# Kernel tuning notes

Measured on AMD Instinct MI355X. Metric: run time of the kernel, lower is better.

## Reference

```python
import jax, jax.numpy as jnp
from jax import lax
import numpy as np


def conv2d(x, w, b=None, stride=1, padding=0, groups=1, dilation=1):
    out = lax.conv_general_dilated(
        x, w, (stride, stride), [(padding, padding)] * 2,
        rhs_dilation=(dilation, dilation), feature_group_count=groups,
        dimension_numbers=('NCHW', 'OIHW', 'NCHW'))
    return out if b is None else out + b[None, :, None, None]


def unfold1d(x, k, axis):
    # torch.nn.functional.unfold with kernel (k,1) or (1,k), pad k//2 on that axis.
    # Returns [B, C, k, H, W] (channel-major, kernel-tap inner), matching torch layout.
    pad = k // 2
    pads = [(0, 0)] * 4
    pads[axis] = (pad, pad)
    xp = jnp.pad(x, pads)
    return jnp.stack([lax.slice_in_dim(xp, i, i + x.shape[axis], axis=axis)
                      for i in range(k)], axis=2)


def ikba(x, att, k, g, b_cb, w_cb):
    # Per-pixel dynamic grouped conv: attention mixes nset codebook kernels,
    # applied as vertical (k,1) then horizontal (1,k) unfold-matmul-fold.
    B, c, H, W = x.shape
    nset = att.shape[1]
    cg = c // g
    P = H * W
    a = att.reshape(B, nset, P).transpose(0, 2, 1)          # [B,P,nset]
    bias = a @ b_cb[0]                                      # [B,P,c]
    attk = a @ w_cb[0]                                      # [B,P, 2*c*cg*k]
    half = attk.shape[-1] // 2
    ah = attk[..., :half].reshape(B, P, g, cg, cg * k)
    aw = attk[..., half:].reshape(B, P, g, cg, cg * k)
    # vertical pass
    ufh = unfold1d(x, k, 2).reshape(B, g, cg * k, P).transpose(0, 3, 1, 2)  # [B,P,g,cg*k]
    xh = jnp.einsum('bpgij,bpgj->bpgi', ah, ufh).reshape(B, P, c)
    xh = xh.transpose(0, 2, 1).reshape(B, c, H, W)
    # horizontal pass
    ufw = unfold1d(xh, k, 3).reshape(B, g, cg * k, P).transpose(0, 3, 1, 2)
    xw = jnp.einsum('bpgij,bpgj->bpgi', aw, ufw).reshape(B, P, c) + bias
    return xw.transpose(0, 2, 1).reshape(B, c, H, W)


def hff_forward(x, dw1_w, dw2_w, proj_w, lka0_w, lkas_w, lka1_w, lka1_b,
                sca_w, sca_b, c1a_w, c1b_w, c2a_w, c2a_b, c2b_w, c2b_b,
                c211_w, c211_b, w_cb, b_cb, attgamma, ga1):
    C = x.shape[1]
    K, GC = 3, 4
    g = C // GC
    sca = conv2d(jnp.mean(x, axis=(2, 3), keepdims=True), sca_w, sca_b)
    x1 = conv2d(conv2d(x, dw1_w), dw2_w, padding=1, groups=C)
    lka = conv2d(conv2d(conv2d(x, lka0_w, padding=2, groups=C),
                        lkas_w, padding=9, groups=C, dilation=3), lka1_w, lka1_b)
    t = conv2d(x, c2a_w, c2a_b, padding=1, groups=c2a_w.shape[0])
    t1, t2 = jnp.split(t, 2, axis=1)  # SimpleGate
    att = conv2d(t1 * t2, c2b_w, c2b_b) * attgamma + conv2d(x, c211_w, c211_b)
    uf = conv2d(conv2d(x, c1a_w), c1b_w, padding=1, groups=C)
    x2 = ikba(uf, att, K, g, b_cb, w_cb) * ga1 + uf
    return conv2d(x1 * x2 * sca * lka, proj_w)


def setup_inputs() -> dict:
    key = jax.random.key(0)
    ks = jax.random.split(key, 24)
    B, C, H, W = 2, 256, 64, 64
    nset, k, gc = 128, 3, 4
    g = C // gc
    cg = C // g
    def rn(i, shape, scale=0.02):
        return jax.random.normal(ks[i], shape, jnp.float32) * scale
    return {
        'x': jax.random.normal(ks[0], (B, C, H, W), jnp.float32),
        'dw1_w': rn(1, (C, C, 1, 1)),
        'dw2_w': rn(2, (C, 1, 3, 3), 0.1),
        'proj_w': rn(3, (C, C, 1, 1)),
        'lka0_w': rn(4, (C, 1, 5, 5), 0.1),
        'lkas_w': rn(5, (C, 1, 7, 7), 0.1),
        'lka1_w': rn(6, (C, C, 1, 1)),
        'lka1_b': rn(7, (C,)),
        'sca_w': rn(8, (C, C, 1, 1)),
        'sca_b': rn(9, (C,)),
        'c1a_w': rn(10, (C, C, 1, 1)),
        'c1b_w': rn(11, (C, 1, 3, 3), 0.1),
        'c2a_w': rn(12, (32, C // 32, 3, 3), 0.1),
        'c2a_b': rn(13, (32,)),
        'c2b_w': rn(14, (nset, 16, 1, 1), 0.1),
        'c2b_b': rn(15, (nset,)),
        'c211_w': rn(16, (nset, C, 1, 1)),
        'c211_b': rn(17, (nset,)),
        'w_cb': rn(18, (1, nset, C * cg * k * 2), 0.05),
        'b_cb': rn(19, (1, nset, C), 0.05),
        'attgamma': jnp.full((1, nset, 1, 1), 0.01, jnp.float32),
        'ga1': jnp.full((1, C, 1, 1), 0.01, jnp.float32),
    }


def reference(x, dw1_w, dw2_w, proj_w, lka0_w, lkas_w, lka1_w, lka1_b,
              sca_w, sca_b, c1a_w, c1b_w, c2a_w, c2a_b, c2b_w, c2b_b,
              c211_w, c211_b, w_cb, b_cb, attgamma, ga1):
    return hff_forward(x, dw1_w, dw2_w, proj_w, lka0_w, lkas_w, lka1_w, lka1_b,
                       sca_w, sca_b, c1a_w, c1b_w, c2a_w, c2a_b, c2b_w, c2b_b,
                       c211_w, c211_b, w_cb, b_cb, attgamma, ga1)
```

## Files before the change

kernel.cpp:

```cpp
#include <hip/hip_runtime.h>
#include <cstddef>

#define P_ 4096
#define HW_ 64

typedef __bf16 bf16x8 __attribute__((ext_vector_type(8)));
typedef float f32x4 __attribute__((ext_vector_type(4)));

__device__ inline ushort f2bf(float f) {
  unsigned u = __float_as_uint(f);
  unsigned r = (u + 0x7FFFu + ((u >> 16) & 1u)) >> 16;
  return (ushort)r;
}
__device__ inline float bf2f(ushort h) {
  return __uint_as_float(((unsigned)h) << 16);
}
__device__ inline unsigned pack2(ushort a, ushort b) {
  return (unsigned)a | ((unsigned)b << 16);
}

__global__ __launch_bounds__(256) void prep_mean_kernel(
    const float* __restrict__ w_cb, const float* __restrict__ dw1_w,
    const float* __restrict__ lka1_w, const float* __restrict__ c1a_w,
    const float* __restrict__ proj_w, const float* __restrict__ c211_w,
    const float* __restrict__ b_cb, ushort* __restrict__ wT,
    ushort* __restrict__ W5h, ushort* __restrict__ W5l,
    ushort* __restrict__ bth, ushort* __restrict__ btl,
    const float* __restrict__ x, float* __restrict__ mean) {
  __shared__ float T[128][65];
  int blk = blockIdx.x;
  int t = threadIdx.x;
  if (blk < 96) {
    int c0 = blk * 64;
#pragma unroll
    for (int i = 0; i < 32; ++i) {
      int l = i * 256 + t;
      int n = l >> 6, c = l & 63;
      T[n][c] = w_cb[(size_t)n * 6144 + c0 + c];
    }
    __syncthreads();
#pragma unroll
    for (int i = 0; i < 4; ++i) {
      int l = i * 256 + t;
      int c = l >> 4, n8 = (l & 15) << 3;
      ushort v[8];
#pragma unroll
      for (int u = 0; u < 8; ++u) v[u] = f2bf(T[n8 + u][c]);
      *(uint4*)&wT[(size_t)(c0 + c) * 128 + n8] = *(uint4*)v;
    }
  } else if (blk < 240) {
    int f = (blk - 96) * 2048 + t * 8;
    const float* srcs[5] = {dw1_w, lka1_w, c1a_w, proj_w, c211_w};
    const int base[6] = {0, 65536, 131072, 196608, 262144, 294912};
    int r = 0;
    while (f >= base[r + 1]) ++r;
    const float* s = srcs[r] + (f - base[r]);
    float4 a = *(const float4*)s;
    float4 b4 = *(const float4*)(s + 4);
    float vv[8] = {a.x, a.y, a.z, a.w, b4.x, b4.y, b4.z, b4.w};
    ushort vh[8], vl[8];
#pragma unroll
    for (int u = 0; u < 8; ++u) {
      ushort h = f2bf(vv[u]);
      vh[u] = h;
      vl[u] = f2bf(vv[u] - bf2f(h));
    }
    *(uint4*)&W5h[f] = *(uint4*)vh;
    *(uint4*)&W5l[f] = *(uint4*)vl;
  } else if (blk < 244) {
    int c0 = (blk - 240) * 64;
#pragma unroll
    for (int i = 0; i < 32; ++i) {
      int l = i * 256 + t;
      int n = l >> 6, c = l & 63;
      T[n][c] = b_cb[(size_t)n * 256 + c0 + c];
    }
    __syncthreads();
#pragma unroll
    for (int i = 0; i < 4; ++i) {
      int l = i * 256 + t;
      int c = l >> 4, n8 = (l & 15) << 3;
      ushort vh[8], vl[8];
#pragma unroll
      for (int u = 0; u < 8; ++u) {
        float fv = T[n8 + u][c];
        ushort h = f2bf(fv);
        vh[u] = h;
        vl[u] = f2bf(fv - bf2f(h));
      }
      *(uint4*)&bth[(size_t)(c0 + c) * 128 + n8] = *(uint4*)vh;
      *(uint4*)&btl[(size_t)(c0 + c) * 128 + n8] = *(uint4*)vl;
    }
  } else {
    int bc = blk - 244;
    const float* xp = x + (size_t)bc * P_;
    float s = 0.f;
    for (int i = t; i < P_; i += 256) s += xp[i];
    float* red = (float*)T;
    red[t] = s;
    __syncthreads();
    for (int off2 = 128; off2 > 0; off2 >>= 1) {
      if (t < off2) red[t] += red[t + off2];
      __syncthreads();
    }
    if (t == 0) mean[bc] = red[0] * (1.f / P_);
  }
}


__device__ inline void xsplit_body(const float* sb, ushort* dhb, ushort* dlb,
                                   int p0, int K, char* smem) {
  float (*T)[65] = (float(*)[65])smem;
  int t = threadIdx.x;
#pragma unroll
  for (int i = 0; i < 32; ++i) {
    int l = i * 256 + t;
    int n = l >> 6, c = l & 63;
    T[n][c] = sb[(size_t)n * P_ + p0 + c];
  }
  __syncthreads();
#pragma unroll
  for (int i = 0; i < 4; ++i) {
    int l = i * 256 + t;
    int c = l >> 4, n8 = (l & 15) << 3;
    ushort vh[8], vl[8];
#pragma unroll
    for (int u = 0; u < 8; ++u) {
      float f = T[n8 + u][c];
      ushort h = f2bf(f);
      vh[u] = h;
      vl[u] = f2bf(f - bf2f(h));
    }
    *(uint4*)&dhb[(size_t)(p0 + c) * K + n8] = *(uint4*)vh;
    *(uint4*)&dlb[(size_t)(p0 + c) * K + n8] = *(uint4*)vl;
  }
}

__device__ inline void gemm_body(const ushort* Whb, const ushort* Wlb,
                                 const ushort* Xhb, const ushort* Xlb,
                                 const float* bias, float* out, int M, int m0,
                                 int p0, int b, int K, char* smem) {
  ushort* Wsh = (ushort*)smem;
  ushort* Wsl = (ushort*)(smem + 9216);
  ushort* Xsh = (ushort*)(smem + 18432);
  ushort* Xsl = (ushort*)(smem + 27648);
  int t = threadIdx.x;
  int w = t >> 6, lane = t & 63, lm = lane & 15, lq = lane >> 4;
  f32x4 C[4];
#pragma unroll
  for (int pt = 0; pt < 4; ++pt) C[pt] = (f32x4)(0.f);
  for (int k0 = 0; k0 < K; k0 += 64) {
#pragma unroll
    for (int i = 0; i < 2; ++i) {
      int u = i * 256 + t;
      int row = u >> 3, k8 = (u & 7) * 8;
      *(uint4*)&Wsh[row * 72 + k8] = *(const uint4*)&Whb[(size_t)row * K + k0 + k8];
      *(uint4*)&Wsl[row * 72 + k8] = *(const uint4*)&Wlb[(size_t)row * K + k0 + k8];
      *(uint4*)&Xsh[row * 72 + k8] = *(const uint4*)&Xhb[(size_t)row * K + k0 + k8];
      *(uint4*)&Xsl[row * 72 + k8] = *(const uint4*)&Xlb[(size_t)row * K + k0 + k8];
    }
    __syncthreads();
#pragma unroll
    for (int kt = 0; kt < 2; ++kt) {
      bf16x8 Ah = *(const bf16x8*)&Wsh[(w * 16 + lm) * 72 + kt * 32 + lq * 8];
      bf16x8 Al = *(const bf16x8*)&Wsl[(w * 16 + lm) * 72 + kt * 32 + lq * 8];
#pragma unroll
      for (int pt = 0; pt < 4; ++pt) {
        bf16x8 Bh = *(const bf16x8*)&Xsh[(pt * 16 + lm) * 72 + kt * 32 + lq * 8];
        bf16x8 Bl = *(const bf16x8*)&Xsl[(pt * 16 + lm) * 72 + kt * 32 + lq * 8];
        C[pt] = __builtin_amdgcn_mfma_f32_16x16x32_bf16(Ah, Bh, C[pt], 0, 0, 0);
        C[pt] = __builtin_amdgcn_mfma_f32_16x16x32_bf16(Al, Bh, C[pt], 0, 0, 0);
        C[pt] = __builtin_amdgcn_mfma_f32_16x16x32_bf16(Ah, Bl, C[pt], 0, 0, 0);
      }
    }
    __syncthreads();
  }
#pragma unroll
  for (int pt = 0; pt < 4; ++pt) {
    int p = p0 + pt * 16 + lm;
#pragma unroll
    for (int r = 0; r < 4; ++r) {
      int m = m0 + w * 16 + lq * 4 + r;
      float v = C[pt][r];
      if (bias) v += bias[m];
      out[((size_t)b * M + m) * P_ + p] = v;
    }
  }
}

__global__ __launch_bounds__(256) void gemm_bf16s_kernel(
    const ushort* __restrict__ Wh, const ushort* __restrict__ Wl,
    const ushort* __restrict__ Xh, const ushort* __restrict__ Xl,
    const float* __restrict__ bias, float* __restrict__ out, int M, int K) {
  __shared__ __align__(16) char smem[36864];
  int p0 = blockIdx.x * 64, m0 = blockIdx.y * 64, b = blockIdx.z;
  gemm_body(Wh + (size_t)m0 * K, Wl + (size_t)m0 * K,
            Xh + ((size_t)b * P_ + p0) * K, Xl + ((size_t)b * P_ + p0) * K,
            bias, out, M, m0, p0, b, K, smem);
}

__global__ __launch_bounds__(256) void sca_xsplit_kernel(
    const float* __restrict__ x, ushort* __restrict__ dh,
    ushort* __restrict__ dl, const float* __restrict__ mean,
    const float* __restrict__ w, const float* __restrict__ bias,
    float* __restrict__ sca) {
  __shared__ __align__(16) char smem[33280];
  int blk = blockIdx.x;
  int t = threadIdx.x;
  if (blk < 256) {
    const int K = 256;
    int p0 = (blk & 63) * 64;
    int kb = (blk >> 6) & 1;
    int b = blk >> 7;
    xsplit_body(x + ((size_t)b * K + kb * 128) * P_,
                dh + (size_t)b * P_ * K + (size_t)kb * 128,
                dl + (size_t)b * P_ * K + (size_t)kb * 128, p0, K, smem);
  } else {
    int b = blk - 256, c = t;
    const float* mb = mean + b * 256;
    const float* wr = w + c * 256;
    float s = bias[c];
    for (int k = 0; k < 256; ++k) s += wr[k] * mb[k];
    sca[b * 256 + c] = s;
  }
}

__global__ __launch_bounds__(256) void main1_kernel(
    const ushort* __restrict__ Xh, const ushort* __restrict__ Xl,
    const ushort* __restrict__ W5h, const ushort* __restrict__ W5l,
    const float* __restrict__ c211_b, float* __restrict__ B1,
    float* __restrict__ B3, float* __restrict__ att0,
    const float* __restrict__ x, const float* __restrict__ w0,
    const float* __restrict__ w1, float* __restrict__ outlka,
    const float* __restrict__ c2aw, const float* __restrict__ c2ab,
    float* __restrict__ sgate) {
  __shared__ __align__(16) char smem[45392];
  int blk = blockIdx.x;
  int t = threadIdx.x;
  if (blk < 1280) {
    const int K = 256;
    int p = blk & 63;
    int my = (blk >> 6) % 10;
    int b = blk / 640;
    const ushort *Wh, *Wl;
    float* out;
    const float* bias = nullptr;
    int M, m0;
    if (my < 4) {
      Wh = W5h; Wl = W5l; out = B1; M = 256; m0 = my * 64;
    } else if (my < 8) {
      Wh = W5h + 131072; Wl = W5l + 131072; out = B3; M = 256; m0 = (my - 4) * 64;
    } else {
      Wh = W5h + 262144; Wl = W5l + 262144; out = att0; M = 128;
      m0 = (my - 8) * 64; bias = c211_b;
    }
    int p0 = p * 64;
    gemm_body(Wh + (size_t)m0 * K, Wl + (size_t)m0 * K,
              Xh + ((size_t)b * P_ + p0) * K, Xl + ((size_t)b * P_ + p0) * K,
              bias, out, M, m0, p0, b, K, smem);
  } else if (blk < 1792) {
    constexpr int PN0 = 68;
    constexpr int PN1 = 82;
    float* p0a = (float*)smem;
    float* p1a = (float*)(smem + PN0 * PN0 * 4);
    int bc = blk - 1280;
    const float* ib = x + (size_t)bc * P_;
    for (int i = t; i < PN0 * PN0; i += 256) p0a[i] = 0.f;
    for (int i = t; i < PN1 * PN1; i += 256) p1a[i] = 0.f;
    __syncthreads();
#pragma unroll
    for (int i = 0; i < 4; ++i) {
      int l = i * 1024 + t * 4;
      int y = l >> 6, xx = l & 63;
      float4 v = *(const float4*)(ib + l);
      float* d = &p0a[(y + 2) * PN0 + 2 + xx];
      d[0] = v.x; d[1] = v.y; d[2] = v.z; d[3] = v.w;
    }
    float wr0[25];
    {
      const float* wp = w0 + (size_t)(bc & 255) * 25;
#pragma unroll
      for (int i = 0; i < 25; ++i) wr0[i] = wp[i];
    }
    __syncthreads();
#pragma unroll
    for (int r = 0; r < 16; ++r) {
      int l = r * 256 + t;
      int y = l >> 6, xx = l & 63;
      float s = 0.f;
#pragma unroll
      for (int dy = 0; dy < 5; ++dy)
#pragma unroll
        for (int dx = 0; dx < 5; ++dx)
          s += wr0[dy * 5 + dx] * p0a[(y + dy) * PN0 + xx + dx];
      p1a[(y + 9) * PN1 + 9 + xx] = s;
    }
    float wr1[49];
    {
      const float* wp = w1 + (size_t)(bc & 255) * 49;
#pragma unroll
      for (int i = 0; i < 49; ++i) wr1[i] = wp[i];
    }
    __syncthreads();
    float* ob = outlka + (size_t)bc * P_;
#pragma unroll
    for (int r = 0; r < 16; ++r) {
      int l = r * 256 + t;
      int y = l >> 6, xx = l & 63;
      float s = 0.f;
#pragma unroll
      for (int dy = 0; dy < 7; ++dy)
#pragma unroll
        for (int dx = 0; dx < 7; ++dx)
          s += wr1[dy * 7 + dx] * p1a[(y + dy * 3) * PN1 + xx + dx * 3];
      ob[l] = s;
    }
  } else {
    int idx = (blk - 1792) * 256 + t;
    int xq = idx & 63, y = (idx >> 6) & 63, go = (idx >> 12) & 15, b = idx >> 16;
    float acc[2];
#pragma unroll
    for (int h = 0; h < 2; ++h) {
      int gc = go + h * 16;
      const float* wr = c2aw + gc * 72;
      const float* xb = x + ((size_t)b * 256 + gc * 8) * P_;
      float ss = c2ab[gc];
      for (int ci = 0; ci < 8; ++ci)
        for (int dy = 0; dy < 3; ++dy) {
          int yy = y + dy - 1;
          if (yy < 0 || yy >= 64) continue;
          for (int dx = 0; dx < 3; ++dx) {
            int xx = xq + dx - 1;
            if (xx < 0 || xx >= 64) continue;
            ss += wr[ci * 9 + dy * 3 + dx] * xb[(size_t)ci * P_ + yy * 64 + xx];
          }
        }
      acc[h] = ss;
    }
    sgate[idx] = acc[0] * acc[1];
  }
}

__global__ __launch_bounds__(256) void dwsplit_kernel(
    const float* __restrict__ in1, const float* __restrict__ w1,
    float* __restrict__ out1, const float* __restrict__ in2,
    const float* __restrict__ w2, float* __restrict__ out2,
    const float* __restrict__ B6, ushort* __restrict__ XT2h,
    ushort* __restrict__ XT2l) {
  __shared__ __align__(16) char smem[33280];
  int blk = blockIdx.x;
  int t = threadIdx.x;
  if (blk < 1024) {
    constexpr int PN = 66;
    float* pl = (float*)smem;
    int which = blk >> 9;
    int bc = blk & 511;
    const float* in = which ? in2 : in1;
    const float* w = which ? w2 : w1;
    float* out = which ? out2 : out1;
    const float* ib = in + (size_t)bc * P_;
    for (int i = t; i < PN * PN; i += 256) pl[i] = 0.f;
    __syncthreads();
#pragma unroll
    for (int i = 0; i < 4; ++i) {
      int l = i * 1024 + t * 4;
      int y = l >> 6, xx = l & 63;
      float4 v = *(const float4*)(ib + l);
      float* d = &pl[(y + 1) * PN + 1 + xx];
      d[0] = v.x; d[1] = v.y; d[2] = v.z; d[3] = v.w;
    }
    float wr[9];
    const float* wp = w + (size_t)(bc & 255) * 9;
#pragma unroll
    for (int i = 0; i < 9; ++i) wr[i] = wp[i];
    __syncthreads();
    float* ob = out + (size_t)bc * P_;
#pragma unroll
    for (int r = 0; r < 16; ++r) {
      int l = r * 256 + t;
      int y = l >> 6, xx = l & 63;
      float s = 0.f;
#pragma unroll
      for (int dy = 0; dy < 3; ++dy)
#pragma unroll
        for (int dx = 0; dx < 3; ++dx)
          s += wr[dy * 3 + dx] * pl[(y + dy) * PN + xx + dx];
      ob[l] = s;
    }
  } else {
    const int K = 256;
    int l = blk - 1024;
    int p0 = (l & 63) * 64;
    int kb = (l >> 6) & 1;
    int b = l >> 7;
    xsplit_body(B6 + ((size_t)b * K + kb * 128) * P_,
                XT2h + (size_t)b * P_ * K + (size_t)kb * 128,
                XT2l + (size_t)b * P_ * K + (size_t)kb * 128, p0, K, smem);
  }
}

__global__ __launch_bounds__(256) void gemm_c2b_kernel(
    const ushort* __restrict__ Wh, const ushort* __restrict__ Wl,
    const ushort* __restrict__ XT2h, const ushort* __restrict__ XT2l,
    const float* __restrict__ lka1_b, float* __restrict__ B1,
    const float* __restrict__ sb, const float* __restrict__ c2bw,
    const float* __restrict__ c2bb, const float* __restrict__ gamma,
    const float* __restrict__ res, ushort* __restrict__ outh,
    ushort* __restrict__ outl) {
  __shared__ __align__(16) char smem[36864];
  int my = blockIdx.y;
  int b = blockIdx.z;
  int t = threadIdx.x;
  if (my < 4) {
    const int K = 256;
    int p0 = blockIdx.x * 64, m0 = my * 64;
    gemm_body(Wh + (size_t)m0 * K, Wl + (size_t)m0 * K,
              XT2h + ((size_t)b * P_ + p0) * K, XT2l + ((size_t)b * P_ + p0) * K,
              lka1_b, B1, 256, m0, p0, b, K, smem);
  } else {
    const int K = 16, M = 128;
    int p0 = blockIdx.x * 64;
    int m0 = (my - 4) * 64;
    float (*Ws)[68] = (float(*)[68])smem;
    float (*Xs)[68] = (float(*)[68])(smem + 4352 * 4);
    int tm = t >> 4, tp = t & 15;
    float acc[4][4] = {};
    const float* inb = sb + (size_t)b * K * P_;
    {
      int kk = t >> 4, pq = (t & 15) << 2;
      float4 v = *(const float4*)(inb + (size_t)kk * P_ + p0 + pq);
      *(float4*)&Xs[kk][pq] = v;
    }
    {
      int mm = t >> 2, kq = (t & 3) << 2;
      float4 v = *(const float4*)(c2bw + (size_t)(m0 + mm) * K + kq);
      Ws[kq + 0][mm] = v.x; Ws[kq + 1][mm] = v.y;
      Ws[kq + 2][mm] = v.z; Ws[kq + 3][mm] = v.w;
    }
    __syncthreads();
#pragma unroll
    for (int kk = 0; kk < 16; ++kk) {
      const float4 wv = *(const float4*)&Ws[kk][tm << 2];
      const float4 xv = *(const float4*)&Xs[kk][tp << 2];
      const float wa[4] = {wv.x, wv.y, wv.z, wv.w};
      const float xa[4] = {xv.x, xv.y, xv.z, xv.w};
#pragma unroll
      for (int i = 0; i < 4; ++i)
#pragma unroll
        for (int j = 0; j < 4; ++j) acc[i][j] += wa[i] * xa[j];
    }
    float val[4][4];
#pragma unroll
    for (int i = 0; i < 4; ++i) {
      int m = m0 + (tm << 2) + i;
      float bv = c2bb[m], gm = gamma[m];
      float4 rv = *(const float4*)(res + ((size_t)b * M + m) * P_ + p0 + (tp << 2));
      val[i][0] = (acc[i][0] + bv) * gm + rv.x;
      val[i][1] = (acc[i][1] + bv) * gm + rv.y;
      val[i][2] = (acc[i][2] + bv) * gm + rv.z;
      val[i][3] = (acc[i][3] + bv) * gm + rv.w;
    }
#pragma unroll
    for (int j = 0; j < 4; ++j) {
      int p = p0 + (tp << 2) + j;
      ushort vh[4], vl[4];
#pragma unroll
      for (int i = 0; i < 4; ++i) {
        float f = val[i][j];
        ushort h = f2bf(f);
        vh[i] = h;
        vl[i] = f2bf(f - bf2f(h));
      }
      size_t a = ((size_t)b * P_ + p) * 128 + m0 + (tm << 2);
      uint2 hv, lv;
      hv.x = pack2(vh[0], vh[1]); hv.y = pack2(vh[2], vh[3]);
      lv.x = pack2(vl[0], vl[1]); lv.y = pack2(vl[2], vl[3]);
      *(uint2*)&outh[a] = hv;
      *(uint2*)&outl[a] = lv;
    }
  }
}

__global__ __launch_bounds__(256) void ikba_mfma_kernel(
    const float* __restrict__ in, const ushort* __restrict__ attT,
    const ushort* __restrict__ Wt, int dirH, int wofs,
    const ushort* __restrict__ bth, const ushort* __restrict__ btl,
    const float* __restrict__ uf_ep, const float* __restrict__ ga1,
    const float* __restrict__ x1, const float* __restrict__ lka,
    const float* __restrict__ sca, ushort* __restrict__ pXh,
    ushort* __restrict__ pXl, float* __restrict__ outV) {
  __shared__ float Ts[2][4][16][66];
  __shared__ float bls[64 * 17];

  int t = threadIdx.x;
  int b = blockIdx.z;
  int quad = blockIdx.y;
  int y = blockIdx.x;
  int p0 = y * 64;
  int gg = t >> 6;
  int lane = t & 63;
  int lm = lane & 15, lq = lane >> 4;
  int gi = quad * 4 + gg;
  int x = lane;

  const ushort* Wbase = Wt + ((size_t)wofs + (size_t)gi * 48) * 128;
  bf16x8 Af[3][4];
#pragma unroll
  for (int ct = 0; ct < 3; ++ct)
#pragma unroll
    for (int K = 0; K < 4; ++K)
      Af[ct][K] = *(const bf16x8*)&Wbase[(ct * 16 + lm) * 128 + K * 32 + lq * 8];

  const ushort* Ab = attT + ((size_t)b * P_ + p0) * 128;
  f32x4 Cf[3][4];
#pragma unroll
  for (int ct = 0; ct < 3; ++ct)
#pragma unroll
    for (int pt = 0; pt < 4; ++pt) Cf[ct][pt] = (f32x4)(0.f);

#pragma unroll
  for (int pt = 0; pt < 4; ++pt) {
    bf16x8 Bf[4];
#pragma unroll
    for (int K = 0; K < 4; ++K)
      Bf[K] = *(const bf16x8*)&Ab[(pt * 16 + lm) * 128 + K * 32 + lq * 8];
#pragma unroll
    for (int ct = 0; ct < 3; ++ct)
#pragma unroll
      for (int K = 0; K < 4; ++K)
        Cf[ct][pt] = __builtin_amdgcn_mfma_f32_16x16x32_bf16(
            Af[ct][K], Bf[K], Cf[ct][pt], 0, 0, 0);
  }

  if (dirH) {
    f32x4 Cb = (f32x4)(0.f);
#pragma unroll
    for (int K = 0; K < 4; ++K) {
      bf16x8 Bb = *(const bf16x8*)&Ab[(gg * 16 + lm) * 128 + K * 32 + lq * 8];
      bf16x8 Abh = *(const bf16x8*)&bth[(size_t)(quad * 16 + lm) * 128 + K * 32 + lq * 8];
      bf16x8 Abl = *(const bf16x8*)&btl[(size_t)(quad * 16 + lm) * 128 + K * 32 + lq * 8];
      Cb = __builtin_amdgcn_mfma_f32_16x16x32_bf16(Abh, Bb, Cb, 0, 0, 0);
      Cb = __builtin_amdgcn_mfma_f32_16x16x32_bf16(Abl, Bb, Cb, 0, 0, 0);
    }
#pragma unroll
    for (int r = 0; r < 4; ++r)
      bls[(gg * 16 + lm) * 17 + lq * 4 + r] = Cb[r];
  }

  float u[12];
  const float* inb = in + ((size_t)b * 256 + gi * 4) * P_;
  if (dirH) {
#pragma unroll
    for (int j = 0; j < 12; ++j) {
      int ci = j / 3, tap = j % 3;
      int xx = x + tap - 1;
      u[j] = (xx >= 0 && xx < 64) ? inb[(size_t)ci * P_ + p0 + xx] : 0.f;
    }
  } else {
#pragma unroll
    for (int j = 0; j < 12; ++j) {
      int ci = j / 3, tap = j % 3;
      int yy = y + tap - 1;
      u[j] = (yy >= 0 && yy < 64) ? inb[(size_t)ci * P_ + yy * 64 + x] : 0.f;
    }
  }

  float s4[4] = {0.f, 0.f, 0.f, 0.f};
#pragma unroll
  for (int ct = 0; ct < 3; ++ct) {
    int bi = ct & 1;
#pragma unroll
    for (int pt = 0; pt < 4; ++pt)
#pragma unroll
      for (int r = 0; r < 4; ++r)
        Ts[bi][gg][lq * 4 + r][pt * 16 + lm] = Cf[ct][pt][r];
    __syncthreads();
#pragma unroll
    for (int cl = 0; cl < 16; ++cl) {
      int col = ct * 16 + cl;
      int i = col / 12, j = col % 12;
      s4[i] += Ts[bi][gg][cl][x] * u[j];
    }
  }

#pragma unroll
  for (int i = 0; i < 4; ++i) {
    int ch = gi * 4 + i;
    size_t oidx = ((size_t)b * 256 + ch) * P_ + p0 + x;
    if (dirH) {
      float biasv = bls[x * 17 + gg * 4 + i];
      float x2v = (s4[i] + biasv) * ga1[ch] + uf_ep[oidx];
      float pr = x1[oidx] * x2v * sca[b * 256 + ch] * lka[oidx];
      ushort h = f2bf(pr);
      ushort lo = f2bf(pr - bf2f(h));
      s4[i] = __uint_as_float(pack2(h, lo));
    } else {
      outV[oidx] = s4[i];
    }
  }
  if (dirH) {
    size_t xa = ((size_t)b * P_ + p0 + x) * 256 + quad * 16 + gg * 4;
    uint2 hv, lv;
    unsigned w0 = __float_as_uint(s4[0]), w1 = __float_as_uint(s4[1]);
    unsigned w2 = __float_as_uint(s4[2]), w3 = __float_as_uint(s4[3]);
    hv.x = (w0 & 0xFFFFu) | ((w1 & 0xFFFFu) << 16);
    hv.y = (w2 & 0xFFFFu) | ((w3 & 0xFFFFu) << 16);
    lv.x = (w0 >> 16) | (w1 & 0xFFFF0000u);
    lv.y = (w2 >> 16) | (w3 & 0xFFFF0000u);
    *(uint2*)&pXh[xa] = hv;
    *(uint2*)&pXl[xa] = lv;
  }
}

extern "C" void kernel_launch(void* const* d_in, const int* in_sizes, int n_in,
                              void* d_out, int out_size, void* d_ws, size_t ws_size,
                              hipStream_t stream) {
  const float* x      = (const float*)d_in[0];
  const float* dw1_w  = (const float*)d_in[1];
  const float* dw2_w  = (const float*)d_in[2];
  const float* proj_w = (const float*)d_in[3];
  const float* lka0_w = (const float*)d_in[4];
  const float* lkas_w = (const float*)d_in[5];
  const float* lka1_w = (const float*)d_in[6];
  const float* lka1_b = (const float*)d_in[7];
  const float* sca_w  = (const float*)d_in[8];
  const float* sca_b  = (const float*)d_in[9];
  const float* c1a_w  = (const float*)d_in[10];
  const float* c1b_w  = (const float*)d_in[11];
  const float* c2a_w  = (const float*)d_in[12];
  const float* c2a_b  = (const float*)d_in[13];
  const float* c2b_w  = (const float*)d_in[14];
  const float* c2b_b  = (const float*)d_in[15];
  const float* c211_w = (const float*)d_in[16];
  const float* c211_b = (const float*)d_in[17];
  const float* w_cb   = (const float*)d_in[18];
  const float* b_cb   = (const float*)d_in[19];
  const float* attg   = (const float*)d_in[20];
  const float* ga1    = (const float*)d_in[21];
  float* out = (float*)d_out;

  const size_t NCHW = 2u * 256u * P_;
  float* ws = (float*)d_ws;
  size_t off = 0;
  float* meanb = ws + off; off += 512;
  float* scab  = ws + off; off += 512;
  float* B1 = ws + off; off += NCHW;
  float* B2 = ws + off; off += NCHW;
  float* B3 = ws + off; off += NCHW;
  float* B4 = ws + off; off += NCHW;
  float* B5 = ws + off; off += NCHW;
  float* B6 = ws + off; off += NCHW;
  float* sb   = ws + off; off += 2u * 16u * P_;
  float* att0 = ws + off; off += 2u * 128u * P_;
  ushort* wT    = (ushort*)(ws + off); off += 393216;
  ushort* W5h   = (ushort*)(ws + off); off += 147456;
  ushort* W5l   = (ushort*)(ws + off); off += 147456;
  ushort* bth   = (ushort*)(ws + off); off += 16384;
  ushort* btl   = (ushort*)(ws + off); off += 16384;
  ushort* XTxh  = (ushort*)(ws + off); off += 1048576;
  ushort* XTxl  = (ushort*)(ws + off); off += 1048576;
  ushort* XT2h  = (ushort*)(ws + off); off += 1048576;
  ushort* XT2l  = (ushort*)(ws + off); off += 1048576;
  ushort* XT3h  = (ushort*)(ws + off); off += 1048576;
  ushort* XT3l  = (ushort*)(ws + off); off += 1048576;
  ushort* attTh = (ushort*)(ws + off); off += 524288;
  ushort* attTl = (ushort*)(ws + off); off += 524288;

  const ushort* Wlka1h = W5h + 65536,  *Wlka1l = W5l + 65536;
  const ushort* Wprojh = W5h + 196608, *Wprojl = W5l + 196608;

  dim3 blk(256);

  prep_mean_kernel<<<756, blk, 0, stream>>>(w_cb, dw1_w, lka1_w, c1a_w, proj_w,
                                            c211_w, b_cb, wT, W5h, W5l, bth, btl,
                                            x, meanb);
  sca_xsplit_kernel<<<258, blk, 0, stream>>>(x, XTxh, XTxl, meanb, sca_w, sca_b,
                                             scab);
  main1_kernel<<<2304, blk, 0, stream>>>(XTxh, XTxl, W5h, W5l, c211_b,
                                         B1, B3, att0, x, lka0_w, lkas_w, B6,
                                         c2a_w, c2a_b, sb);
  dwsplit_kernel<<<1280, blk, 0, stream>>>(B1, dw2_w, B2, B3, c1b_w, B5,
                                           B6, XT2h, XT2l);
  gemm_c2b_kernel<<<dim3(64, 6, 2), blk, 0, stream>>>(
      Wlka1h, Wlka1l, XT2h, XT2l, lka1_b, B1,
      sb, c2b_w, c2b_b, attg, att0, attTh, attTl);
  dim3 gik(64, 16, 2);
  ikba_mfma_kernel<<<gik, blk, 0, stream>>>(B5, attTh, wT, 0, 0, nullptr, nullptr,
                                            nullptr, nullptr, nullptr, nullptr,
                                            nullptr, nullptr, nullptr, B4);
  ikba_mfma_kernel<<<gik, blk, 0, stream>>>(B4, attTh, wT, 1, 3072, bth, btl,
                                            B5, ga1, B2, B1, scab, XT3h, XT3l,
                                            nullptr);
  gemm_bf16s_kernel<<<dim3(64, 4, 2), blk, 0, stream>>>(Wprojh, Wprojl, XT3h,
                                                        XT3l, nullptr, out, 256, 256);
}
```

Measured before the change: 272.4 us.

## Merge xsplit into prep kernel, fold sca into main1, register-tile depthwise convs

Moves the x transpose-split work into the prep kernel and the SCA matvec into main1, removing one kernel launch. Rewrites the 5x5, dilated 7x7 and 3x3 depthwise convolutions so each thread computes a 4x4 output tile from float4 row loads in shared memory, reusing loaded inputs across outputs instead of doing scalar per-pixel loads. It also reorders main1 so the conv blocks are dispatched before the GEMM blocks. Weights are now read from global memory inside the loop rather than preloaded into registers, and shared memory use grows slightly.

```diff
diff --git a/kernel.cpp b/kernel.cpp
--- a/kernel.cpp
+++ b/kernel.cpp
@@ -19,15 +19,98 @@
   return (unsigned)a | ((unsigned)b << 16);
 }
 
-__global__ __launch_bounds__(256) void prep_mean_kernel(
+
+__device__ inline void xsplit_body(const float* sb, ushort* dhb, ushort* dlb,
+                                   int p0, int K, char* smem) {
+  float (*T)[65] = (float(*)[65])smem;
+  int t = threadIdx.x;
+#pragma unroll
+  for (int i = 0; i < 32; ++i) {
+    int l = i * 256 + t;
+    int n = l >> 6, c = l & 63;
+    T[n][c] = sb[(size_t)n * P_ + p0 + c];
+  }
+  __syncthreads();
+#pragma unroll
+  for (int i = 0; i < 4; ++i) {
+    int l = i * 256 + t;
+    int c = l >> 4, n8 = (l & 15) << 3;
+    ushort vh[8], vl[8];
+#pragma unroll
+    for (int u = 0; u < 8; ++u) {
+      float f = T[n8 + u][c];
+      ushort h = f2bf(f);
+      vh[u] = h;
+      vl[u] = f2bf(f - bf2f(h));
+    }
+    *(uint4*)&dhb[(size_t)(p0 + c) * K + n8] = *(uint4*)vh;
+    *(uint4*)&dlb[(size_t)(p0 + c) * K + n8] = *(uint4*)vl;
+  }
+}
+
+__device__ inline void gemm_body(const ushort* Whb, const ushort* Wlb,
+                                 const ushort* Xhb, const ushort* Xlb,
+                                 const float* bias, float* out, int M, int m0,
+                                 int p0, int b, int K, char* smem) {
+  ushort* Wsh = (ushort*)smem;
+  ushort* Wsl = (ushort*)(smem + 9216);
+  ushort* Xsh = (ushort*)(smem + 18432);
+  ushort* Xsl = (ushort*)(smem + 27648);
+  int t = threadIdx.x;
+  int w = t >> 6, lane = t & 63, lm = lane & 15, lq = lane >> 4;
+  f32x4 C[4];
+#pragma unroll
+  for (int pt = 0; pt < 4; ++pt) C[pt] = (f32x4)(0.f);
+  for (int k0 = 0; k0 < K; k0 += 64) {
+#pragma unroll
+    for (int i = 0; i < 2; ++i) {
+      int u = i * 256 + t;
+      int row = u >> 3, k8 = (u & 7) * 8;
+      *(uint4*)&Wsh[row * 72 + k8] = *(const uint4*)&Whb[(size_t)row * K + k0 + k8];
+      *(uint4*)&Wsl[row * 72 + k8] = *(const uint4*)&Wlb[(size_t)row * K + k0 + k8];
+      *(uint4*)&Xsh[row * 72 + k8] = *(const uint4*)&Xhb[(size_t)row * K + k0 + k8];
+      *(uint4*)&Xsl[row * 72 + k8] = *(const uint4*)&Xlb[(size_t)row * K + k0 + k8];
+    }
+    __syncthreads();
+#pragma unroll
+    for (int kt = 0; kt < 2; ++kt) {
+      bf16x8 Ah = *(const bf16x8*)&Wsh[(w * 16 + lm) * 72 + kt * 32 + lq * 8];
+      bf16x8 Al = *(const bf16x8*)&Wsl[(w * 16 + lm) * 72 + kt * 32 + lq * 8];
+#pragma unroll
+      for (int pt = 0; pt < 4; ++pt) {
+        bf16x8 Bh = *(const bf16x8*)&Xsh[(pt * 16 + lm) * 72 + kt * 32 + lq * 8];
+        bf16x8 Bl = *(const bf16x8*)&Xsl[(pt * 16 + lm) * 72 + kt * 32 + lq * 8];
+        C[pt] = __builtin_amdgcn_mfma_f32_16x16x32_bf16(Ah, Bh, C[pt], 0, 0, 0);
+        C[pt] = __builtin_amdgcn_mfma_f32_16x16x32_bf16(Al, Bh, C[pt], 0, 0, 0);
+        C[pt] = __builtin_amdgcn_mfma_f32_16x16x32_bf16(Ah, Bl, C[pt], 0, 0, 0);
+      }
+    }
+    __syncthreads();
+  }
+#pragma unroll
+  for (int pt = 0; pt < 4; ++pt) {
+    int p = p0 + pt * 16 + lm;
+#pragma unroll
+    for (int r = 0; r < 4; ++r) {
+      int m = m0 + w * 16 + lq * 4 + r;
+      float v = C[pt][r];
+      if (bias) v += bias[m];
+      out[((size_t)b * M + m) * P_ + p] = v;
+    }
+  }
+}
+
+__global__ __launch_bounds__(256) void prep_kernel(
     const float* __restrict__ w_cb, const float* __restrict__ dw1_w,
     const float* __restrict__ lka1_w, const float* __restrict__ c1a_w,
     const float* __restrict__ proj_w, const float* __restrict__ c211_w,
     const float* __restrict__ b_cb, ushort* __restrict__ wT,
     ushort* __restrict__ W5h, ushort* __restrict__ W5l,
     ushort* __restrict__ bth, ushort* __restrict__ btl,
-    const float* __restrict__ x, float* __restrict__ mean) {
-  __shared__ float T[128][65];
+    const float* __restrict__ x, float* __restrict__ mean,
+    ushort* __restrict__ XTxh, ushort* __restrict__ XTxl) {
+  __shared__ __align__(16) char smem[33280];
+  float (*T)[65] = (float(*)[65])smem;
   int blk = blockIdx.x;
   int t = threadIdx.x;
   if (blk < 96) {
@@ -91,12 +174,12 @@
       *(uint4*)&bth[(size_t)(c0 + c) * 128 + n8] = *(uint4*)vh;
       *(uint4*)&btl[(size_t)(c0 + c) * 128 + n8] = *(uint4*)vl;
     }
-  } else {
+  } else if (blk < 756) {
     int bc = blk - 244;
     const float* xp = x + (size_t)bc * P_;
     float s = 0.f;
     for (int i = t; i < P_; i += 256) s += xp[i];
-    float* red = (float*)T;
+    float* red = (float*)smem;
     red[t] = s;
     __syncthreads();
     for (int off2 = 128; off2 > 0; off2 >>= 1) {
@@ -104,124 +187,15 @@
       __syncthreads();
     }
     if (t == 0) mean[bc] = red[0] * (1.f / P_);
-  }
-}
-
-
-__device__ inline void xsplit_body(const float* sb, ushort* dhb, ushort* dlb,
-                                   int p0, int K, char* smem) {
-  float (*T)[65] = (float(*)[65])smem;
-  int t = threadIdx.x;
-#pragma unroll
-  for (int i = 0; i < 32; ++i) {
-    int l = i * 256 + t;
-    int n = l >> 6, c = l & 63;
-    T[n][c] = sb[(size_t)n * P_ + p0 + c];
-  }
-  __syncthreads();
-#pragma unroll
-  for (int i = 0; i < 4; ++i) {
-    int l = i * 256 + t;
-    int c = l >> 4, n8 = (l & 15) << 3;
-    ushort vh[8], vl[8];
-#pragma unroll
-    for (int u = 0; u < 8; ++u) {
-      float f = T[n8 + u][c];
-      ushort h = f2bf(f);
-      vh[u] = h;
-      vl[u] = f2bf(f - bf2f(h));
-    }
-    *(uint4*)&dhb[(size_t)(p0 + c) * K + n8] = *(uint4*)vh;
-    *(uint4*)&dlb[(size_t)(p0 + c) * K + n8] = *(uint4*)vl;
-  }
-}
-
-__device__ inline void gemm_body(const ushort* Whb, const ushort* Wlb,
-                                 const ushort* Xhb, const ushort* Xlb,
-                                 const float* bias, float* out, int M, int m0,
-                                 int p0, int b, int K, char* smem) {
-  ushort* Wsh = (ushort*)smem;
-  ushort* Wsl = (ushort*)(smem + 9216);
-  ushort* Xsh = (ushort*)(smem + 18432);
-  ushort* Xsl = (ushort*)(smem + 27648);
-  int t = threadIdx.x;
-  int w = t >> 6, lane = t & 63, lm = lane & 15, lq = lane >> 4;
-  f32x4 C[4];
-#pragma unroll
-  for (int pt = 0; pt < 4; ++pt) C[pt] = (f32x4)(0.f);
-  for (int k0 = 0; k0 < K; k0 += 64) {
-#pragma unroll
-    for (int i = 0; i < 2; ++i) {
-      int u = i * 256 + t;
-      int row = u >> 3, k8 = (u & 7) * 8;
-      *(uint4*)&Wsh[row * 72 + k8] = *(const uint4*)&Whb[(size_t)row * K + k0 + k8];
-      *(uint4*)&Wsl[row * 72 + k8] = *(const uint4*)&Wlb[(size_t)row * K + k0 + k8];
-      *(uint4*)&Xsh[row * 72 + k8] = *(const uint4*)&Xhb[(size_t)row * K + k0 + k8];
-      *(uint4*)&Xsl[row * 72 + k8] = *(const uint4*)&Xlb[(size_t)row * K + k0 + k8];
-    }
-    __syncthreads();
-#pragma unroll
-    for (int kt = 0; kt < 2; ++kt) {
-      bf16x8 Ah = *(const bf16x8*)&Wsh[(w * 16 + lm) * 72 + kt * 32 + lq * 8];
-      bf16x8 Al = *(const bf16x8*)&Wsl[(w * 16 + lm) * 72 + kt * 32 + lq * 8];
-#pragma unroll
-      for (int pt = 0; pt < 4; ++pt) {
-        bf16x8 Bh = *(const bf16x8*)&Xsh[(pt * 16 + lm) * 72 + kt * 32 + lq * 8];
-        bf16x8 Bl = *(const bf16x8*)&Xsl[(pt * 16 + lm) * 72 + kt * 32 + lq * 8];
-        C[pt] = __builtin_amdgcn_mfma_f32_16x16x32_bf16(Ah, Bh, C[pt], 0, 0, 0);
-        C[pt] = __builtin_amdgcn_mfma_f32_16x16x32_bf16(Al, Bh, C[pt], 0, 0, 0);
-        C[pt] = __builtin_amdgcn_mfma_f32_16x16x32_bf16(Ah, Bl, C[pt], 0, 0, 0);
-      }
-    }
-    __syncthreads();
-  }
-#pragma unroll
-  for (int pt = 0; pt < 4; ++pt) {
-    int p = p0 + pt * 16 + lm;
-#pragma unroll
-    for (int r = 0; r < 4; ++r) {
-      int m = m0 + w * 16 + lq * 4 + r;
-      float v = C[pt][r];
-      if (bias) v += bias[m];
-      out[((size_t)b * M + m) * P_ + p] = v;
-    }
-  }
-}
-
-__global__ __launch_bounds__(256) void gemm_bf16s_kernel(
-    const ushort* __restrict__ Wh, const ushort* __restrict__ Wl,
-    const ushort* __restrict__ Xh, const ushort* __restrict__ Xl,
-    const float* __restrict__ bias, float* __restrict__ out, int M, int K) {
-  __shared__ __align__(16) char smem[36864];
-  int p0 = blockIdx.x * 64, m0 = blockIdx.y * 64, b = blockIdx.z;
-  gemm_body(Wh + (size_t)m0 * K, Wl + (size_t)m0 * K,
-            Xh + ((size_t)b * P_ + p0) * K, Xl + ((size_t)b * P_ + p0) * K,
-            bias, out, M, m0, p0, b, K, smem);
-}
-
-__global__ __launch_bounds__(256) void sca_xsplit_kernel(
-    const float* __restrict__ x, ushort* __restrict__ dh,
-    ushort* __restrict__ dl, const float* __restrict__ mean,
-    const float* __restrict__ w, const float* __restrict__ bias,
-    float* __restrict__ sca) {
-  __shared__ __align__(16) char smem[33280];
-  int blk = blockIdx.x;
-  int t = threadIdx.x;
-  if (blk < 256) {
+  } else {
     const int K = 256;
-    int p0 = (blk & 63) * 64;
-    int kb = (blk >> 6) & 1;
-    int b = blk >> 7;
+    int l = blk - 756;
+    int p0 = (l & 63) * 64;
+    int kb = (l >> 6) & 1;
+    int b = l >> 7;
     xsplit_body(x + ((size_t)b * K + kb * 128) * P_,
-                dh + (size_t)b * P_ * K + (size_t)kb * 128,
-                dl + (size_t)b * P_ * K + (size_t)kb * 128, p0, K, smem);
-  } else {
-    int b = blk - 256, c = t;
-    const float* mb = mean + b * 256;
-    const float* wr = w + c * 256;
-    float s = bias[c];
-    for (int k = 0; k < 256; ++k) s += wr[k] * mb[k];
-    sca[b * 256 + c] = s;
+                XTxh + (size_t)b * P_ * K + (size_t)kb * 128,
+                XTxl + (size_t)b * P_ * K + (size_t)kb * 128, p0, K, smem);
   }
 }
 
@@ -233,90 +207,94 @@
     const float* __restrict__ x, const float* __restrict__ w0,
     const float* __restrict__ w1, float* __restrict__ outlka,
     const float* __restrict__ c2aw, const float* __restrict__ c2ab,
-    float* __restrict__ sgate) {
-  __shared__ __align__(16) char smem[45392];
+    float* __restrict__ sgate, const float* __restrict__ mean,
+    const float* __restrict__ sca_w, const float* __restrict__ sca_b,
+    float* __restrict__ sca) {
+  __shared__ __align__(16) char smem[48448];
   int blk = blockIdx.x;
   int t = threadIdx.x;
-  if (blk < 1280) {
-    const int K = 256;
-    int p = blk & 63;
-    int my = (blk >> 6) % 10;
-    int b = blk / 640;
-    const ushort *Wh, *Wl;
-    float* out;
-    const float* bias = nullptr;
-    int M, m0;
-    if (my < 4) {
-      Wh = W5h; Wl = W5l; out = B1; M = 256; m0 = my * 64;
-    } else if (my < 8) {
-      Wh = W5h + 131072; Wl = W5l + 131072; out = B3; M = 256; m0 = (my - 4) * 64;
-    } else {
-      Wh = W5h + 262144; Wl = W5l + 262144; out = att0; M = 128;
-      m0 = (my - 8) * 64; bias = c211_b;
-    }
-    int p0 = p * 64;
-    gemm_body(Wh + (size_t)m0 * K, Wl + (size_t)m0 * K,
-              Xh + ((size_t)b * P_ + p0) * K, Xl + ((size_t)b * P_ + p0) * K,
-              bias, out, M, m0, p0, b, K, smem);
-  } else if (blk < 1792) {
-    constexpr int PN0 = 68;
-    constexpr int PN1 = 82;
+  if (blk < 512) {
     float* p0a = (float*)smem;
-    float* p1a = (float*)(smem + PN0 * PN0 * 4);
-    int bc = blk - 1280;
+    float* p1a = (float*)(smem + 19584);
+    int bc = blk;
     const float* ib = x + (size_t)bc * P_;
-    for (int i = t; i < PN0 * PN0; i += 256) p0a[i] = 0.f;
-    for (int i = t; i < PN1 * PN1; i += 256) p1a[i] = 0.f;
+    const float* wp0 = w0 + (size_t)(bc & 255) * 25;
+    const float* wp1 = w1 + (size_t)(bc & 255) * 49;
+    for (int i = t; i < 4896; i += 256) p0a[i] = 0.f;
+    for (int i = t; i < 7216; i += 256) p1a[i] = 0.f;
     __syncthreads();
 #pragma unroll
     for (int i = 0; i < 4; ++i) {
       int l = i * 1024 + t * 4;
       int y = l >> 6, xx = l & 63;
-      float4 v = *(const float4*)(ib + l);
-      float* d = &p0a[(y + 2) * PN0 + 2 + xx];
-      d[0] = v.x; d[1] = v.y; d[2] = v.z; d[3] = v.w;
-    }
-    float wr0[25];
+      *(float4*)&p0a[(y + 2) * 72 + 4 + xx] = *(const float4*)(ib + l);
+    }
+    __syncthreads();
+    int x0 = (t & 15) * 4, y0 = (t >> 4) * 4;
     {
-      const float* wp = w0 + (size_t)(bc & 255) * 25;
-#pragma unroll
-      for (int i = 0; i < 25; ++i) wr0[i] = wp[i];
-    }
-    __syncthreads();
-#pragma unroll
-    for (int r = 0; r < 16; ++r) {
-      int l = r * 256 + t;
-      int y = l >> 6, xx = l & 63;
-      float s = 0.f;
-#pragma unroll
-      for (int dy = 0; dy < 5; ++dy)
-#pragma unroll
-        for (int dx = 0; dx < 5; ++dx)
-          s += wr0[dy * 5 + dx] * p0a[(y + dy) * PN0 + xx + dx];
-      p1a[(y + 9) * PN1 + 9 + xx] = s;
-    }
-    float wr1[49];
+      float acc[4][4] = {};
+#pragma unroll
+      for (int ry = 0; ry < 8; ++ry) {
+        const float* row = &p0a[(y0 + ry) * 72 + x0];
+        float4 v0 = *(const float4*)row;
+        float4 v1 = *(const float4*)(row + 4);
+        float4 v2 = *(const float4*)(row + 8);
+        float rv[12] = {v0.x, v0.y, v0.z, v0.w, v1.x, v1.y, v1.z, v1.w,
+                        v2.x, v2.y, v2.z, v2.w};
+#pragma unroll
+        for (int oy = 0; oy < 4; ++oy) {
+          int dy = ry - oy;
+          if (dy >= 0 && dy <= 4) {
+#pragma unroll
+            for (int dx = 0; dx < 5; ++dx) {
+              float wv = wp0[dy * 5 + dx];
+#pragma unroll
+              for (int ox = 0; ox < 4; ++ox)
+                acc[oy][ox] += wv * rv[2 + ox + dx];
+            }
+          }
+        }
+      }
+#pragma unroll
+      for (int oy = 0; oy < 4; ++oy) {
+        float4 v = {acc[oy][0], acc[oy][1], acc[oy][2], acc[oy][3]};
+        *(float4*)&p1a[(y0 + oy + 9) * 88 + 12 + x0] = v;
+      }
+    }
+    __syncthreads();
     {
-      const float* wp = w1 + (size_t)(bc & 255) * 49;
-#pragma unroll
-      for (int i = 0; i < 49; ++i) wr1[i] = wp[i];
-    }
-    __syncthreads();
-    float* ob = outlka + (size_t)bc * P_;
-#pragma unroll
-    for (int r = 0; r < 16; ++r) {
-      int l = r * 256 + t;
-      int y = l >> 6, xx = l & 63;
-      float s = 0.f;
-#pragma unroll
-      for (int dy = 0; dy < 7; ++dy)
-#pragma unroll
-        for (int dx = 0; dx < 7; ++dx)
-          s += wr1[dy * 7 + dx] * p1a[(y + dy * 3) * PN1 + xx + dx * 3];
-      ob[l] = s;
-    }
-  } else {
-    int idx = (blk - 1792) * 256 + t;
+      float acc[4][4] = {};
+#pragma unroll
+      for (int ry = 0; ry < 22; ++ry) {
+        const float* row = &p1a[(y0 + ry) * 88 + x0];
+        float rv[28];
+#pragma unroll
+        for (int q = 0; q < 7; ++q)
+          *(float4*)&rv[q * 4] = *(const float4*)(row + q * 4);
+#pragma unroll
+        for (int oy = 0; oy < 4; ++oy) {
+          int d = ry - oy;
+          if (d >= 0 && d <= 18 && (d % 3) == 0) {
+            int dy = d / 3;
+#pragma unroll
+            for (int dx = 0; dx < 7; ++dx) {
+              float wv = wp1[dy * 7 + dx];
+#pragma unroll
+              for (int ox = 0; ox < 4; ++ox)
+                acc[oy][ox] += wv * rv[3 + ox + 3 * dx];
+            }
+          }
+        }
+      }
+      float* ob = outlka + (size_t)bc * P_;
+#pragma unroll
+      for (int oy = 0; oy < 4; ++oy) {
+        float4 v = {acc[oy][0], acc[oy][1], acc[oy][2], acc[oy][3]};
+        *(float4*)&ob[(y0 + oy) * 64 + x0] = v;
+      }
+    }
+  } else if (blk < 1024) {
+    int idx = (blk - 512) * 256 + t;
     int xq = idx & 63, y = (idx >> 6) & 63, go = (idx >> 12) & 15, b = idx >> 16;
     float acc[2];
 #pragma unroll
@@ -338,6 +316,35 @@
       acc[h] = ss;
     }
     sgate[idx] = acc[0] * acc[1];
+  } else if (blk < 1026) {
+    int b = blk - 1024, c = t;
+    const float* mb = mean + b * 256;
+    const float* wr = sca_w + c * 256;
+    float s = sca_b[c];
+    for (int k = 0; k < 256; ++k) s += wr[k] * mb[k];
+    sca[b * 256 + c] = s;
+  } else {
+    const int K = 256;
+    int g = blk - 1026;
+    int p = g & 63;
+    int my = (g >> 6) % 10;
+    int b = g / 640;
+    const ushort *Wh, *Wl;
+    float* out;
+    const float* bias = nullptr;
+    int M, m0;
+    if (my < 4) {
+      Wh = W5h; Wl = W5l; out = B1; M = 256; m0 = my * 64;
+    } else if (my < 8) {
+      Wh = W5h + 131072; Wl = W5l + 131072; out = B3; M = 256; m0 = (my - 4) * 64;
+    } else {
+      Wh = W5h + 262144; Wl = W5l + 262144; out = att0; M = 128;
+      m0 = (my - 8) * 64; bias = c211_b;
+    }
+    int p0 = p * 64;
+    gemm_body(Wh + (size_t)m0 * K, Wl + (size_t)m0 * K,
+              Xh + ((size_t)b * P_ + p0) * K, Xl + ((size_t)b * P_ + p0) * K,
+              bias, out, M, m0, p0, b, K, smem);
   }
 }
 
@@ -351,7 +358,6 @@
   int blk = blockIdx.x;
   int t = threadIdx.x;
   if (blk < 1024) {
-    constexpr int PN = 66;
     float* pl = (float*)smem;
     int which = blk >> 9;
     int bc = blk & 511;
@@ -359,33 +365,45 @@
     const float* w = which ? w2 : w1;
     float* out = which ? out2 : out1;
     const float* ib = in + (size_t)bc * P_;
-    for (int i = t; i < PN * PN; i += 256) pl[i] = 0.f;
+    const float* wp = w + (size_t)(bc & 255) * 9;
+    for (int i = t; i < 4752; i += 256) pl[i] = 0.f;
     __syncthreads();
 #pragma unroll
     for (int i = 0; i < 4; ++i) {
       int l = i * 1024 + t * 4;
       int y = l >> 6, xx = l & 63;
-      float4 v = *(const float4*)(ib + l);
-      float* d = &pl[(y + 1) * PN + 1 + xx];
-      d[0] = v.x; d[1] = v.y; d[2] = v.z; d[3] = v.w;
-    }
-    float wr[9];
-    const float* wp = w + (size_t)(bc & 255) * 9;
-#pragma unroll
-    for (int i = 0; i < 9; ++i) wr[i] = wp[i];
-    __syncthreads();
+      *(float4*)&pl[(y + 1) * 72 + 4 + xx] = *(const float4*)(ib + l);
+    }
+    __syncthreads();
+    int x0 = (t & 15) * 4, y0 = (t >> 4) * 4;
+    float acc[4][4] = {};
+#pragma unroll
+    for (int ry = 0; ry < 6; ++ry) {
+      const float* row = &pl[(y0 + ry) * 72 + x0];
+      float4 v0 = *(const float4*)row;
+      float4 v1 = *(const float4*)(row + 4);
+      float4 v2 = *(const float4*)(row + 8);
+      float rv[12] = {v0.x, v0.y, v0.z, v0.w, v1.x, v1.y, v1.z, v1.w,
+                      v2.x, v2.y, v2.z, v2.w};
+#pragma unroll
+      for (int oy = 0; oy < 4; ++oy) {
+        int dy = ry - oy;
+        if (dy >= 0 && dy <= 2) {
+#pragma unroll
+          for (int dx = 0; dx < 3; ++dx) {
+            float wv = wp[dy * 3 + dx];
+#pragma unroll
+            for (int ox = 0; ox < 4; ++ox)
+              acc[oy][ox] += wv * rv[3 + ox + dx];
+          }
+        }
+      }
+    }
     float* ob = out + (size_t)bc * P_;
 #pragma unroll
-    for (int r = 0; r < 16; ++r) {
-      int l = r * 256 + t;
-      int y = l >> 6, xx = l & 63;
-      float s = 0.f;
-#pragma unroll
-      for (int dy = 0; dy < 3; ++dy)
-#pragma unroll
-        for (int dx = 0; dx < 3; ++dx)
-          s += wr[dy * 3 + dx] * pl[(y + dy) * PN + xx + dx];
-      ob[l] = s;
+    for (int oy = 0; oy < 4; ++oy) {
+      float4 v = {acc[oy][0], acc[oy][1], acc[oy][2], acc[oy][3]};
+      *(float4*)&ob[(y0 + oy) * 64 + x0] = v;
     }
   } else {
     const int K = 256;
@@ -612,6 +630,17 @@
   }
 }
 
+__global__ __launch_bounds__(256) void gemm_bf16s_kernel(
+    const ushort* __restrict__ Wh, const ushort* __restrict__ Wl,
+    const ushort* __restrict__ Xh, const ushort* __restrict__ Xl,
+    const float* __restrict__ bias, float* __restrict__ out, int M, int K) {
+  __shared__ __align__(16) char smem[36864];
+  int p0 = blockIdx.x * 64, m0 = blockIdx.y * 64, b = blockIdx.z;
+  gemm_body(Wh + (size_t)m0 * K, Wl + (size_t)m0 * K,
+            Xh + ((size_t)b * P_ + p0) * K, Xl + ((size_t)b * P_ + p0) * K,
+            bias, out, M, m0, p0, b, K, smem);
+}
+
 extern "C" void kernel_launch(void* const* d_in, const int* in_sizes, int n_in,
                               void* d_out, int out_size, void* d_ws, size_t ws_size,
                               hipStream_t stream) {
@@ -671,14 +700,13 @@
 
   dim3 blk(256);
 
-  prep_mean_kernel<<<756, blk, 0, stream>>>(w_cb, dw1_w, lka1_w, c1a_w, proj_w,
-                                            c211_w, b_cb, wT, W5h, W5l, bth, btl,
-                                            x, meanb);
-  sca_xsplit_kernel<<<258, blk, 0, stream>>>(x, XTxh, XTxl, meanb, sca_w, sca_b,
-                                             scab);
-  main1_kernel<<<2304, blk, 0, stream>>>(XTxh, XTxl, W5h, W5l, c211_b,
+  prep_kernel<<<1012, blk, 0, stream>>>(w_cb, dw1_w, lka1_w, c1a_w, proj_w,
+                                        c211_w, b_cb, wT, W5h, W5l, bth, btl,
+                                        x, meanb, XTxh, XTxl);
+  main1_kernel<<<2306, blk, 0, stream>>>(XTxh, XTxl, W5h, W5l, c211_b,
                                          B1, B3, att0, x, lka0_w, lkas_w, B6,
-                                         c2a_w, c2a_b, sb);
+                                         c2a_w, c2a_b, sb, meanb, sca_w, sca_b,
+                                         scab);
   dwsplit_kernel<<<1280, blk, 0, stream>>>(B1, dw2_w, B2, B3, c1b_w, B5,
                                            B6, XT2h, XT2l);
   gemm_c2b_kernel<<<dim3(64, 6, 2), blk, 0, stream>>>(
```

Result: faster. 266.6 us (-2.1%).
